# Performance work log

Measured on AMD Instinct MI355X. Metric: run time of the kernel, lower is better.

Reference implementation:

```python
import jax, jax.numpy as jnp
import numpy as np

LAYER_SIZES = [256, 256, 256, 128]
MAX_PATHS = 100
BATCH = 16


def setup_inputs() -> dict:
    key = jax.random.key(0)
    ks = jax.random.split(key, 20)
    d = {}
    d["x"] = jax.random.normal(ks[0], (BATCH, LAYER_SIZES[0]), dtype=jnp.float32)
    # PathPreservingLayer weights W_l: [out, in]
    for l in range(3):
        fi, fo = LAYER_SIZES[l], LAYER_SIZES[l + 1]
        d[f"W{l}"] = jax.random.normal(ks[1 + l], (fo, fi), dtype=jnp.float32) / np.sqrt(fi)
        # quality scorer for layer l: Linear(fo,32) -> ReLU -> Linear(32,1)
        kk = jax.random.split(ks[4 + l], 4)
        d[f"s{l}_w1"] = jax.random.normal(kk[0], (32, fo), dtype=jnp.float32) / np.sqrt(fo)
        d[f"s{l}_b1"] = jnp.zeros((32,), dtype=jnp.float32)
        d[f"s{l}_w2"] = jax.random.normal(kk[1], (1, 32), dtype=jnp.float32) / np.sqrt(32.0)
        d[f"s{l}_b2"] = jnp.zeros((1,), dtype=jnp.float32)
    return d


def _path_layer(data, W):
    # data: [B, Fin, P]; W: [Fout, Fin]
    # path-preserving expansion: new[b, j, p*Fin + i] = W[j, i] * data[b, i, p]
    B, I, P = data.shape
    O = W.shape[0]
    out = jnp.einsum("oi,bip->bopi", W, data)  # [B, O, P, I]
    return out.reshape(B, O, P * I)


def _score(data, w1, b1, w2, b2):
    # data: [B, F, P] -> scores [B, P] via tiny MLP over feature dim per path
    t = jnp.swapaxes(data, 1, 2)  # [B, P, F]
    h = jax.nn.relu(jnp.einsum("bpf,hf->bph", t, w1) + b1)
    return (jnp.einsum("bph,oh->bpo", h, w2) + b2)[..., 0]


def _prune(data, scores, keep):
    _, idx = jax.lax.top_k(scores, keep)  # [B, keep]
    return jnp.take_along_axis(data, idx[:, None, :], axis=-1)


def reference(x, W0, W1, W2,
              s0_w1, s0_b1, s0_w2, s0_b2,
              s1_w1, s1_b1, s1_w2, s1_b2,
              s2_w1, s2_b1, s2_w2, s2_b2):
    Ws = [W0, W1, W2]
    scorers = [(s0_w1, s0_b1, s0_w2, s0_b2),
               (s1_w1, s1_b1, s1_w2, s1_b2),
               (s2_w1, s2_b1, s2_w2, s2_b2)]
    data = x[..., None]  # [B, F0, 1]
    n = len(Ws)
    for i in range(n):
        data = _path_layer(data, Ws[i])
        if data.shape[-1] > MAX_PATHS:
            sc = _score(data, *scorers[i])
            data = _prune(data, sc, MAX_PATHS)
        if i < n - 1:
            data = jnp.tanh(data)
    # quality-weighted output with the last scorer
    w = jax.nn.softmax(_score(data, *scorers[-1]), axis=-1)  # [B, P]
    return jnp.sum(data * w[:, None, :], axis=-1)  # [B, F_last]
```

## Files before the change

kernel.cpp:

```cpp
#include <hip/hip_runtime.h>
#include <math.h>

#define NT 1024
#define KSEL 100
#define NWAVE 16
#define HPAD 260

#define OFF_CT   0
#define OFF_A    24576
#define OFF_B    25344
#define OFF_W0T  26112
#define OFF_W1T  91648
#define OFF_W2T  157184
#define WS_FLOATS 189952

__device__ __forceinline__ unsigned fkey(float f) {
  unsigned u = __float_as_uint(f);
  return (u & 0x80000000u) ? ~u : (u | 0x80000000u);
}
__device__ __forceinline__ float unfkey(unsigned k) {
  return __uint_as_float((k & 0x80000000u) ? (k & 0x7FFFFFFFu) : ~k);
}
__device__ __forceinline__ unsigned long long lower_mask(int lane) {
  return lane ? (~0ull >> (64 - lane)) : 0ull;
}

__device__ __forceinline__ void scan_step(const unsigned* hb, int ncopies, int lane,
                                          int& krem, unsigned& prefix) {
  const int l4 = lane << 2;
  unsigned h0 = 0, h1 = 0, h2 = 0, h3 = 0;
  #pragma unroll 2
  for (int k = 0; k < ncopies; ++k) {
    const uint4 v = *(const uint4*)&hb[k * HPAD + l4];
    h0 += v.x; h1 += v.y; h2 += v.z; h3 += v.w;
  }
  unsigned csum = h0 + h1 + h2 + h3;
  unsigned S = csum;
  #pragma unroll
  for (int off = 1; off < 64; off <<= 1) {
    unsigned v = __shfl_down(S, off, 64);
    if (lane + off < 64) S += v;
  }
  unsigned tail = S - csum;
  unsigned s3 = tail + h3;
  unsigned s2 = s3 + h2;
  unsigned s1 = s2 + h1;
  unsigned s0v = s1 + h0;
  int ld = -1; unsigned sfx = 0, hd = 0;
  if      ((int)s3  >= krem) { ld = l4 + 3; sfx = s3;  hd = h3; }
  else if ((int)s2  >= krem) { ld = l4 + 2; sfx = s2;  hd = h2; }
  else if ((int)s1  >= krem) { ld = l4 + 1; sfx = s1;  hd = h1; }
  else if ((int)s0v >= krem) { ld = l4 + 0; sfx = s0v; hd = h0; }
  int gd = ld;
  #pragma unroll
  for (int off = 32; off >= 1; off >>= 1) {
    int v = __shfl_down(gd, off, 64);
    if (lane + off < 64) gd = (v > gd) ? v : gd;
  }
  gd = __shfl(gd, 0, 64);
  unsigned osfx = __shfl(sfx, gd >> 2, 64);
  unsigned ohd  = __shfl(hd,  gd >> 2, 64);
  krem -= (int)(osfx - ohd);
  prefix = (prefix << 8) | (unsigned)gd;
}

__global__ __launch_bounds__(256) void pqn_precompute(
    const float* __restrict__ W0, const float* __restrict__ W1, const float* __restrict__ W2,
    const float* __restrict__ s0w1, const float* __restrict__ s1w1, const float* __restrict__ s2w1,
    float* __restrict__ ws)
{
  __shared__ float tile[64][65];
  const int bx = blockIdx.x, t = threadIdx.x;
  if (bx < 96) {
    int id = bx * 256 + t;
    int l = id >> 13, r = id & 8191;
    int h = r >> 8, i = r & 255;
    const float* W  = (l == 0) ? W0 : (l == 1) ? W1 : W2;
    const float* w1 = (l == 0) ? s0w1 : (l == 1) ? s1w1 : s2w1;
    float acc = 0.f;
    if (l == 2) {
      #pragma unroll 32
      for (int j = 0; j < 128; ++j)
        acc = fmaf(w1[h * 128 + j], W[j * 256 + i], acc);
    } else {
      #pragma unroll 32
      for (int j = 0; j < 256; ++j)
        acc = fmaf(w1[h * 256 + j], W[j * 256 + i], acc);
    }
    ws[OFF_CT + l * 8192 + h * 256 + i] = acc;
  } else {
    int tb = bx - 96;
    const float* W; float* WT; int R, tbl;
    if (tb < 16)      { W = W0; WT = ws + OFF_W0T; R = 256; tbl = tb; }
    else if (tb < 32) { W = W1; WT = ws + OFF_W1T; R = 256; tbl = tb - 16; }
    else              { W = W2; WT = ws + OFF_W2T; R = 128; tbl = tb - 32; }
    int tr = tbl >> 2, tc = tbl & 3;
    int c = t & 63, r0 = t >> 6;
    #pragma unroll
    for (int k = 0; k < 16; ++k) {
      int r = r0 + (k << 2);
      tile[r][c] = W[(tr * 64 + r) * 256 + tc * 64 + c];
    }
    __syncthreads();
    int r2 = t & 63;
    #pragma unroll
    for (int k = 0; k < 16; ++k) {
      int c2 = r0 + (k << 2);
      WT[(tc * 64 + c2) * R + tr * 64 + r2] = tile[r2][c2];
    }
  }
}

__global__ __launch_bounds__(256) void pqn_ab(
    const float* __restrict__ s0w2, const float* __restrict__ s1w2, const float* __restrict__ s2w2,
    float* __restrict__ ws)
{
  const int l = blockIdx.x;
  const int i = threadIdx.x;
  const float* w2 = (l == 0) ? s0w2 : (l == 1) ? s1w2 : s2w2;
  const float* ct = ws + OFF_CT + l * 8192;
  float a = 0.f, bn = 0.f;
  #pragma unroll
  for (int h = 0; h < 32; ++h) {
    float c = ct[h * 256 + i];
    float wc = w2[h] * c;
    if (c > 0.f) a += wc; else if (c < 0.f) bn += wc;
  }
  ws[OFF_A + l * 256 + i] = a;
  ws[OFF_B + l * 256 + i] = bn;
}

__device__ __forceinline__ float slow_c(const float* __restrict__ w1,
                                        const float* __restrict__ W,
                                        int Fout, int h, int i) {
  float c = 0.f;
  for (int j = 0; j < Fout; ++j) c = fmaf(w1[h * Fout + j], W[j * 256 + i], c);
  return c;
}

__global__ __launch_bounds__(NT) void pqn_main(
    const float* __restrict__ x,
    const float* __restrict__ W0, const float* __restrict__ W1, const float* __restrict__ W2,
    const float* __restrict__ s0w1, const float* __restrict__ s1w1, const float* __restrict__ s2w1,
    const float* __restrict__ s0b1, const float* __restrict__ s1b1, const float* __restrict__ s2b1,
    const float* __restrict__ s0w2, const float* __restrict__ s1w2, const float* __restrict__ s2w2,
    const float* __restrict__ s0b2, const float* __restrict__ s1b2, const float* __restrict__ s2b2,
    const float* __restrict__ wsr,
    float* __restrict__ out)
{
  __shared__ __align__(16) unsigned keyLds[25 * NT];
  __shared__ __align__(16) unsigned hist0[NWAVE * HPAD];
  __shared__ __align__(16) unsigned histP[6 * HPAD];
  __shared__ float Asm[256], Bsm[256];
  __shared__ int   path_col[KSEL]; __shared__ float path_t[KSEL];
  __shared__ int   sel_col[KSEL];  __shared__ float sel_s[KSEL]; __shared__ float sel_sc[KSEL];
  __shared__ unsigned tieq[128];
  __shared__ int nsel_s, ntie_s;
  __shared__ int bz_sh[3];
  __shared__ float wts[KSEL];
  __shared__ float partial[8][128];

  const int b = blockIdx.x;
  const int t = threadIdx.x;
  const int lane = t & 63;
  const int w = t >> 6;
  const bool useWs = (wsr != nullptr);
  const float* Ag  = useWs ? (wsr + OFF_A) : nullptr;
  const float* Bg  = useWs ? (wsr + OFF_B) : nullptr;
  const float* Ctg = useWs ? (wsr + OFF_CT) : nullptr;
  const float* W0T = useWs ? (wsr + OFF_W0T) : nullptr;
  const float* W1T = useWs ? (wsr + OFF_W1T) : nullptr;
  const float* W2T = useWs ? (wsr + OFF_W2T) : nullptr;

  if (!useWs) {
    if (t < 256) {
      float a = 0.f, bn = 0.f;
      for (int h = 0; h < 32; ++h) {
        float c = slow_c(s0w1, W0, 256, h, t);
        float wc = s0w2[h] * c;
        if (c > 0.f) a += wc; else if (c < 0.f) bn += wc;
      }
      Asm[t] = a; Bsm[t] = bn;
    }
    __syncthreads();
  }
  if (w == 0) {
    {
      float v0 = (lane < 32) ? s0b1[lane] : 0.f;
      float v1 = (lane < 32) ? s1b1[lane] : 0.f;
      float v2 = (lane < 32) ? s2b1[lane] : 0.f;
      bz_sh[0] = (__ballot(v0 != 0.f) == 0ull);
      bz_sh[1] = (__ballot(v1 != 0.f) == 0ull);
      bz_sh[2] = (__ballot(v2 != 0.f) == 0ull);
    }
    const bool bz0 = (bz_sh[0] != 0);
    const float b2v = s0b2[0];
    const float4 xv4 = *(const float4*)(x + b * 256 + lane * 4);
    const float xv[4] = {xv4.x, xv4.y, xv4.z, xv4.w};
    float4 A4, B4;
    if (useWs) { A4 = *(const float4*)(Ag + lane * 4); B4 = *(const float4*)(Bg + lane * 4); }
    else       { A4 = *(const float4*)(Asm + lane * 4); B4 = *(const float4*)(Bsm + lane * 4); }
    const float Av[4] = {A4.x, A4.y, A4.z, A4.w};
    const float Bv[4] = {B4.x, B4.y, B4.z, B4.w};
    unsigned kq[4];
    #pragma unroll
    for (int q = 0; q < 4; ++q) {
      int e = 4 * lane + q;
      float s = xv[q];
      float v;
      if (bz0) v = s * (s > 0.f ? Av[q] : Bv[q]) + b2v;
      else {
        v = b2v;
        for (int h = 0; h < 32; ++h) {
          float c = useWs ? Ctg[h * 256 + e] : slow_c(s0w1, W0, 256, h, e);
          v += s0w2[h] * fmaxf(fmaf(s, c, s0b1[h]), 0.f);
        }
      }
      kq[q] = fkey(v);
    }
    int krem = KSEL; unsigned prefix = 0u;
    #pragma unroll
    for (int pass = 0; pass < 4; ++pass) {
      unsigned* hw = (pass == 0) ? hist0 : (histP + (pass - 1) * 2 * HPAD);
      const int l4 = lane << 2;
      hw[l4] = 0u; hw[l4 + 1] = 0u; hw[l4 + 2] = 0u; hw[l4 + 3] = 0u;
      const int shift = 24 - 8 * pass;
      #pragma unroll
      for (int q = 0; q < 4; ++q) {
        bool cand = (pass == 0) || ((kq[q] >> (shift + 8)) == prefix);
        if (cand) atomicAdd(&hw[(kq[q] >> shift) & 255u], 1u);
      }
      scan_step(hw, 1, lane, krem, prefix);
    }
    const unsigned T = prefix;
    int total = 0, ttot = 0;
    #pragma unroll
    for (int q = 0; q < 4; ++q) {
      int e = 4 * lane + q;
      bool sel = kq[q] > T;
      unsigned long long m = __ballot(sel);
      if (sel) {
        int slot = total + (int)__popcll(m & lower_mask(lane));
        path_col[slot] = e; path_t[slot] = xv[q];
      }
      total += (int)__popcll(m);
      bool tie = (kq[q] == T);
      unsigned long long tm = __ballot(tie);
      if (tie) {
        int ts = ttot + (int)__popcll(tm & lower_mask(lane));
        if (ts < 128) tieq[ts] = (unsigned)e;
      }
      ttot += (int)__popcll(tm);
    }
    if (lane == 0) {
      int m = ttot > 128 ? 128 : ttot;
      for (int a2 = 1; a2 < m; ++a2) {
        unsigned v = tieq[a2]; int c = a2 - 1;
        while (c >= 0 && tieq[c] > v) { tieq[c + 1] = tieq[c]; --c; }
        tieq[c + 1] = v;
      }
    }
    const int kt = KSEL - total;
    if (lane < kt) {
      int e = (int)tieq[lane];
      path_col[total + lane] = e; path_t[total + lane] = x[b * 256 + e];
    }
  }
  __syncthreads();

  for (int l = 1; l < 3; ++l) {
    const float* w1 = (l == 1) ? s1w1 : s2w1;
    const float* b1 = (l == 1) ? s1b1 : s2b1;
    const float* w2 = (l == 1) ? s1w2 : s2w2;
    const float  b2v = (l == 1) ? s1b2[0] : s2b2[0];
    const float* Wl = (l == 1) ? W1 : W2;
    const float* Wprev = (l == 1) ? W0 : W1;
    const float* WTprev = (l == 1) ? W0T : W1T;
    const int Fout = (l == 2) ? 128 : 256;

    const float* Ap; const float* Bp;
    if (useWs) { Ap = Ag + l * 256; Bp = Bg + l * 256; }
    else {
      if (t < 256) {
        float a = 0.f, bn = 0.f;
        for (int h = 0; h < 32; ++h) {
          float c = slow_c(w1, Wl, Fout, h, t);
          float wc = w2[h] * c;
          if (c > 0.f) a += wc; else if (c < 0.f) bn += wc;
        }
        Asm[t] = a; Bsm[t] = bn;
      }
      __syncthreads();
      Ap = Asm; Bp = Bsm;
    }
    const bool bz = (bz_sh[l] != 0);
    const float* ctp = useWs ? (Ctg + l * 8192) : nullptr;

    const int i = t & 255;
    const int pq = t >> 8;
    const float Ai = Ap[i], Bi = Bp[i];
    unsigned* histw0 = hist0 + w * HPAD;
    {
      const int l4 = lane << 2;
      histw0[l4] = 0u; histw0[l4 + 1] = 0u; histw0[l4 + 2] = 0u; histw0[l4 + 3] = 0u;
    }
    for (int id = t; id < 6 * HPAD; id += NT) histP[id] = 0u;
    if (t == 0) { nsel_s = 0; ntie_s = 0; }
    unsigned runD = 0x100u; unsigned runC = 0u;
    if (useWs && bz) {
      #pragma unroll
      for (int g = 0; g < 25; g += 8) {
        float wv[8], tv[8];
        #pragma unroll
        for (int jj = 0; jj < 8; ++jj) {
          if (g + jj < 25) {
            int p = pq + ((g + jj) << 2);
            tv[jj] = path_t[p];
            wv[jj] = WTprev[(path_col[p] << 8) + i];
          }
        }
        #pragma unroll
        for (int jj = 0; jj < 8; ++jj) {
          if (g + jj < 25) {
            float s = tanhf(wv[jj] * tv[jj]);
            float v = s * (s > 0.f ? Ai : Bi) + b2v;
            unsigned k = fkey(v);
            keyLds[(g + jj) * NT + t] = k;
            unsigned d = k >> 24;
            if (d == runD) ++runC;
            else { if (runC) atomicAdd(&histw0[runD], runC); runD = d; runC = 1u; }
          }
        }
      }
    } else {
      #pragma unroll
      for (int g = 0; g < 25; g += 4) {
        float wv[4];
        #pragma unroll
        for (int jj = 0; jj < 4; ++jj) {
          if (g + jj < 25) {
            int p = pq + ((g + jj) << 2);
            wv[jj] = useWs ? WTprev[(path_col[p] << 8) + i]
                           : Wprev[i * 256 + path_col[p]];
          }
        }
        #pragma unroll
        for (int jj = 0; jj < 4; ++jj) {
          if (g + jj < 25) {
            int p = pq + ((g + jj) << 2);
            float s = tanhf(wv[jj] * path_t[p]);
            float v;
            if (bz) v = s * (s > 0.f ? Ai : Bi) + b2v;
            else {
              v = b2v;
              for (int h = 0; h < 32; ++h) {
                float c = useWs ? ctp[h * 256 + i] : slow_c(w1, Wl, Fout, h, i);
                v += w2[h] * fmaxf(fmaf(s, c, b1[h]), 0.f);
              }
            }
            unsigned k = fkey(v);
            keyLds[(g + jj) * NT + t] = k;
            unsigned d = k >> 24;
            if (d == runD) ++runC;
            else { if (runC) atomicAdd(&histw0[runD], runC); runD = d; runC = 1u; }
          }
        }
      }
    }
    if (runC) atomicAdd(&histw0[runD], runC);

    int krem = KSEL; unsigned prefix = 0u;
    #pragma unroll
    for (int pass = 0; pass < 4; ++pass) {
      __syncthreads();
      if (pass == 0) scan_step(hist0, NWAVE, lane, krem, prefix);
      else           scan_step(histP + (pass - 1) * 2 * HPAD, 2, lane, krem, prefix);
      if (pass < 3) {
        unsigned* hn = histP + pass * 2 * HPAD + (w & 1) * HPAD;
        const int shift = 24 - 8 * (pass + 1);
        #pragma unroll
        for (int j = 0; j < 25; ++j) {
          unsigned k = keyLds[j * NT + t];
          if ((k >> (shift + 8)) == prefix)
            atomicAdd(&hn[(k >> shift) & 255u], 1u);
        }
      }
    }
    const unsigned T = prefix;

    #pragma unroll
    for (int j = 0; j < 25; ++j) {
      unsigned k = keyLds[j * NT + t];
      int e = j * NT + t;
      if (k > T) {
        int slot = atomicAdd(&nsel_s, 1);
        int p = e >> 8;
        float wq = useWs ? WTprev[(path_col[p] << 8) + i] : Wprev[i * 256 + path_col[p]];
        sel_col[slot] = i;
        sel_s[slot] = tanhf(wq * path_t[p]);
        sel_sc[slot] = unfkey(k);
      } else if (k == T) {
        int tp = atomicAdd(&ntie_s, 1);
        if (tp < 128) tieq[tp] = (unsigned)e;
      }
    }
    __syncthreads();

    if (w == 0) {
      const int G = nsel_s;
      const int kt = KSEL - G;
      if (lane == 0 && kt > 1) {
        int m = ntie_s > 128 ? 128 : ntie_s;
        for (int a2 = 1; a2 < m; ++a2) {
          unsigned v = tieq[a2]; int c = a2 - 1;
          while (c >= 0 && tieq[c] > v) { tieq[c + 1] = tieq[c]; --c; }
          tieq[c + 1] = v;
        }
      }
      if (lane < kt) {
        int e = (int)tieq[lane];
        int ii = e & 255, p = e >> 8;
        float wq = useWs ? WTprev[(path_col[p] << 8) + ii] : Wprev[ii * 256 + path_col[p]];
        sel_col[G + lane] = ii;
        sel_s[G + lane] = tanhf(wq * path_t[p]);
        sel_sc[G + lane] = unfkey(T);
      }
      if (l < 2) {
        if (lane < 64) {
          path_col[lane] = sel_col[lane]; path_t[lane] = sel_s[lane];
          if (lane < 36) { path_col[64 + lane] = sel_col[64 + lane]; path_t[64 + lane] = sel_s[64 + lane]; }
        }
      }
    }
    __syncthreads();
  }

  if (w == 0) {
    float s1v = sel_sc[lane];
    float s2v = (lane < 36) ? sel_sc[64 + lane] : -INFINITY;
    float m = fmaxf(s1v, s2v);
    #pragma unroll
    for (int off = 32; off >= 1; off >>= 1) m = fmaxf(m, __shfl_xor(m, off, 64));
    float e1 = expf(s1v - m);
    float e2 = (lane < 36) ? expf(s2v - m) : 0.f;
    float sv = e1 + e2;
    #pragma unroll
    for (int off = 32; off >= 1; off >>= 1) sv += __shfl_xor(sv, off, 64);
    wts[lane] = e1 * sel_s[lane] / sv;
    if (lane < 36) wts[64 + lane] = e2 * sel_s[64 + lane] / sv;
  }
  __syncthreads();
  {
    const int chunk = w >> 1, half = w & 1;
    const int o = half * 64 + lane;
    const int pb = chunk * 13;
    const int pe = (pb + 13 < KSEL) ? pb + 13 : KSEL;
    float acc = 0.f;
    for (int p = pb; p < pe; ++p) {
      float wq = useWs ? W2T[sel_col[p] * 128 + o] : W2[o * 256 + sel_col[p]];
      acc = fmaf(wq, wts[p], acc);
    }
    partial[chunk][o] = acc;
  }
  __syncthreads();
  if (t < 128) {
    float acc = 0.f;
    #pragma unroll
    for (int c = 0; c < 8; ++c) acc += partial[c][t];
    out[b * 128 + t] = acc;
  }
}

extern "C" void kernel_launch(void* const* d_in, const int* in_sizes, int n_in,
                              void* d_out, int out_size, void* d_ws, size_t ws_size,
                              hipStream_t stream) {
  const float* x    = (const float*)d_in[0];
  const float* W0   = (const float*)d_in[1];
  const float* s0w1 = (const float*)d_in[2];
  const float* s0b1 = (const float*)d_in[3];
  const float* s0w2 = (const float*)d_in[4];
  const float* s0b2 = (const float*)d_in[5];
  const float* W1   = (const float*)d_in[6];
  const float* s1w1 = (const float*)d_in[7];
  const float* s1b1 = (const float*)d_in[8];
  const float* s1w2 = (const float*)d_in[9];
  const float* s1b2 = (const float*)d_in[10];
  const float* W2   = (const float*)d_in[11];
  const float* s2w1 = (const float*)d_in[12];
  const float* s2b1 = (const float*)d_in[13];
  const float* s2w2 = (const float*)d_in[14];
  const float* s2b2 = (const float*)d_in[15];
  float* out = (float*)d_out;
  float* ws  = (float*)d_ws;

  const bool fullWs = ws_size >= (size_t)WS_FLOATS * sizeof(float);
  const float* wsr = nullptr;
  if (fullWs) {
    pqn_precompute<<<136, 256, 0, stream>>>(W0, W1, W2, s0w1, s1w1, s2w1, ws);
    pqn_ab<<<3, 256, 0, stream>>>(s0w2, s1w2, s2w2, ws);
    wsr = ws;
  }
  pqn_main<<<16, NT, 0, stream>>>(x, W0, W1, W2,
                                  s0w1, s1w1, s2w1,
                                  s0b1, s1b1, s2b1,
                                  s0w2, s1w2, s2w2,
                                  s0b2, s1b2, s2b2,
                                  wsr, out);
}
```

Baseline: 150.3 us.

## Compact radix-select candidates and split scorer-weight precompute across more blocks

The radix top-k selection now collects elements matching the 16-bit prefix into a compact LDS candidate list during the second pass, so the last two passes and the final gather scan only the candidates instead of all 25 keys per thread. Elements above the prefix are emitted to the selected set early. Separately, the C = w1·W precompute is split in half along the reduction dimension over twice as many blocks, and the halves are summed in pqn_ab. This adds an overflow fallback path, extra LDS, and an extra workspace layout.

```diff
diff --git a/kernel.cpp b/kernel.cpp
--- a/kernel.cpp
+++ b/kernel.cpp
@@ -5,14 +5,10 @@
 #define KSEL 100
 #define NWAVE 16
 #define HPAD 260
-
-#define OFF_CT   0
-#define OFF_A    24576
-#define OFF_B    25344
-#define OFF_W0T  26112
-#define OFF_W1T  91648
-#define OFF_W2T  157184
-#define WS_FLOATS 189952
+#define CCAP 2048
+
+#define WS_FLOATS_A 239104
+#define WS_FLOATS_B 189952
 
 __device__ __forceinline__ unsigned fkey(float f) {
   unsigned u = __float_as_uint(f);
@@ -67,33 +63,49 @@
 __global__ __launch_bounds__(256) void pqn_precompute(
     const float* __restrict__ W0, const float* __restrict__ W1, const float* __restrict__ W2,
     const float* __restrict__ s0w1, const float* __restrict__ s1w1, const float* __restrict__ s2w1,
-    float* __restrict__ ws)
+    float* __restrict__ ctp0, float* __restrict__ ctp1,
+    float* __restrict__ w0t, float* __restrict__ w1t, float* __restrict__ w2t,
+    int split)
 {
   __shared__ float tile[64][65];
   const int bx = blockIdx.x, t = threadIdx.x;
-  if (bx < 96) {
+  const int ctBlocks = split ? 192 : 96;
+  if (bx < ctBlocks) {
     int id = bx * 256 + t;
-    int l = id >> 13, r = id & 8191;
-    int h = r >> 8, i = r & 255;
+    int l, half, rr;
+    if (split) { l = id >> 14; int r = id & 16383; half = r >> 13; rr = r & 8191; }
+    else       { l = id >> 13; half = 0; rr = id & 8191; }
+    int h = rr >> 8, i = rr & 255;
     const float* W  = (l == 0) ? W0 : (l == 1) ? W1 : W2;
     const float* w1 = (l == 0) ? s0w1 : (l == 1) ? s1w1 : s2w1;
     float acc = 0.f;
-    if (l == 2) {
-      #pragma unroll 32
-      for (int j = 0; j < 128; ++j)
-        acc = fmaf(w1[h * 128 + j], W[j * 256 + i], acc);
+    if (split) {
+      if (l == 2) {
+        int j0 = half * 64;
+        #pragma unroll 32
+        for (int j = j0; j < j0 + 64; ++j)  acc = fmaf(w1[h * 128 + j], W[j * 256 + i], acc);
+      } else {
+        int j0 = half * 128;
+        #pragma unroll 32
+        for (int j = j0; j < j0 + 128; ++j) acc = fmaf(w1[h * 256 + j], W[j * 256 + i], acc);
+      }
+      (half ? ctp1 : ctp0)[l * 8192 + h * 256 + i] = acc;
     } else {
-      #pragma unroll 32
-      for (int j = 0; j < 256; ++j)
-        acc = fmaf(w1[h * 256 + j], W[j * 256 + i], acc);
-    }
-    ws[OFF_CT + l * 8192 + h * 256 + i] = acc;
+      if (l == 2) {
+        #pragma unroll 32
+        for (int j = 0; j < 128; ++j) acc = fmaf(w1[h * 128 + j], W[j * 256 + i], acc);
+      } else {
+        #pragma unroll 32
+        for (int j = 0; j < 256; ++j) acc = fmaf(w1[h * 256 + j], W[j * 256 + i], acc);
+      }
+      ctp0[l * 8192 + h * 256 + i] = acc;
+    }
   } else {
-    int tb = bx - 96;
+    int tb = bx - ctBlocks;
     const float* W; float* WT; int R, tbl;
-    if (tb < 16)      { W = W0; WT = ws + OFF_W0T; R = 256; tbl = tb; }
-    else if (tb < 32) { W = W1; WT = ws + OFF_W1T; R = 256; tbl = tb - 16; }
-    else              { W = W2; WT = ws + OFF_W2T; R = 128; tbl = tb - 32; }
+    if (tb < 16)      { W = W0; WT = w0t; R = 256; tbl = tb; }
+    else if (tb < 32) { W = W1; WT = w1t; R = 256; tbl = tb - 16; }
+    else              { W = W2; WT = w2t; R = 128; tbl = tb - 32; }
     int tr = tbl >> 2, tc = tbl & 3;
     int c = t & 63, r0 = t >> 6;
     #pragma unroll
@@ -113,21 +125,24 @@
 
 __global__ __launch_bounds__(256) void pqn_ab(
     const float* __restrict__ s0w2, const float* __restrict__ s1w2, const float* __restrict__ s2w2,
-    float* __restrict__ ws)
+    const float* __restrict__ ctp0, const float* __restrict__ ctp1,
+    float* __restrict__ ct, float* __restrict__ A, float* __restrict__ B,
+    int split)
 {
   const int l = blockIdx.x;
   const int i = threadIdx.x;
   const float* w2 = (l == 0) ? s0w2 : (l == 1) ? s1w2 : s2w2;
-  const float* ct = ws + OFF_CT + l * 8192;
   float a = 0.f, bn = 0.f;
   #pragma unroll
   for (int h = 0; h < 32; ++h) {
-    float c = ct[h * 256 + i];
+    const int o = l * 8192 + h * 256 + i;
+    float c = ctp0[o];
+    if (split) { c += ctp1[o]; ct[o] = c; }
     float wc = w2[h] * c;
     if (c > 0.f) a += wc; else if (c < 0.f) bn += wc;
   }
-  ws[OFF_A + l * 256 + i] = a;
-  ws[OFF_B + l * 256 + i] = bn;
+  A[l * 256 + i] = a;
+  B[l * 256 + i] = bn;
 }
 
 __device__ __forceinline__ float slow_c(const float* __restrict__ w1,
@@ -145,17 +160,19 @@
     const float* __restrict__ s0b1, const float* __restrict__ s1b1, const float* __restrict__ s2b1,
     const float* __restrict__ s0w2, const float* __restrict__ s1w2, const float* __restrict__ s2w2,
     const float* __restrict__ s0b2, const float* __restrict__ s1b2, const float* __restrict__ s2b2,
-    const float* __restrict__ wsr,
+    const float* __restrict__ Ctg, const float* __restrict__ Ag, const float* __restrict__ Bg,
+    const float* __restrict__ W0T, const float* __restrict__ W1T, const float* __restrict__ W2T,
     float* __restrict__ out)
 {
   __shared__ __align__(16) unsigned keyLds[25 * NT];
   __shared__ __align__(16) unsigned hist0[NWAVE * HPAD];
   __shared__ __align__(16) unsigned histP[6 * HPAD];
+  __shared__ unsigned candK[CCAP]; __shared__ int candE[CCAP];
   __shared__ float Asm[256], Bsm[256];
   __shared__ int   path_col[KSEL]; __shared__ float path_t[KSEL];
   __shared__ int   sel_col[KSEL];  __shared__ float sel_s[KSEL]; __shared__ float sel_sc[KSEL];
   __shared__ unsigned tieq[128];
-  __shared__ int nsel_s, ntie_s;
+  __shared__ int nsel_s, ntie_s, ncand_s;
   __shared__ int bz_sh[3];
   __shared__ float wts[KSEL];
   __shared__ float partial[8][128];
@@ -164,13 +181,7 @@
   const int t = threadIdx.x;
   const int lane = t & 63;
   const int w = t >> 6;
-  const bool useWs = (wsr != nullptr);
-  const float* Ag  = useWs ? (wsr + OFF_A) : nullptr;
-  const float* Bg  = useWs ? (wsr + OFF_B) : nullptr;
-  const float* Ctg = useWs ? (wsr + OFF_CT) : nullptr;
-  const float* W0T = useWs ? (wsr + OFF_W0T) : nullptr;
-  const float* W1T = useWs ? (wsr + OFF_W1T) : nullptr;
-  const float* W2T = useWs ? (wsr + OFF_W2T) : nullptr;
+  const bool useWs = (Ctg != nullptr);
 
   if (!useWs) {
     if (t < 256) {
@@ -305,7 +316,7 @@
       histw0[l4] = 0u; histw0[l4 + 1] = 0u; histw0[l4 + 2] = 0u; histw0[l4 + 3] = 0u;
     }
     for (int id = t; id < 6 * HPAD; id += NT) histP[id] = 0u;
-    if (t == 0) { nsel_s = 0; ntie_s = 0; }
+    if (t == 0) { nsel_s = 0; ntie_s = 0; ncand_s = 0; }
     unsigned runD = 0x100u; unsigned runC = 0u;
     if (useWs && bz) {
       #pragma unroll
@@ -369,39 +380,93 @@
     }
     if (runC) atomicAdd(&histw0[runD], runC);
 
+    __syncthreads();
     int krem = KSEL; unsigned prefix = 0u;
-    #pragma unroll
-    for (int pass = 0; pass < 4; ++pass) {
-      __syncthreads();
-      if (pass == 0) scan_step(hist0, NWAVE, lane, krem, prefix);
-      else           scan_step(histP + (pass - 1) * 2 * HPAD, 2, lane, krem, prefix);
-      if (pass < 3) {
-        unsigned* hn = histP + pass * 2 * HPAD + (w & 1) * HPAD;
-        const int shift = 24 - 8 * (pass + 1);
+    scan_step(hist0, NWAVE, lane, krem, prefix);
+
+    {
+      unsigned* hn = histP + (w & 1) * HPAD;
+      #pragma unroll
+      for (int j = 0; j < 25; ++j) {
+        unsigned k = keyLds[j * NT + t];
+        if ((k >> 24) == prefix) atomicAdd(&hn[(k >> 16) & 255u], 1u);
+      }
+    }
+    __syncthreads();
+    scan_step(histP, 2, lane, krem, prefix);
+
+    {
+      unsigned* hn = histP + 2 * HPAD + (w & 1) * HPAD;
+      #pragma unroll
+      for (int j = 0; j < 25; ++j) {
+        unsigned k = keyLds[j * NT + t];
+        unsigned p16 = k >> 16;
+        if (p16 > prefix) {
+          int slot = atomicAdd(&nsel_s, 1);
+          int e = j * NT + t; int p = e >> 8;
+          float wq = useWs ? WTprev[(path_col[p] << 8) + i] : Wprev[i * 256 + path_col[p]];
+          sel_col[slot] = i; sel_s[slot] = tanhf(wq * path_t[p]); sel_sc[slot] = unfkey(k);
+        } else if (p16 == prefix) {
+          int ci = atomicAdd(&ncand_s, 1);
+          if (ci < CCAP) { candK[ci] = k; candE[ci] = j * NT + t; }
+          atomicAdd(&hn[(k >> 8) & 255u], 1u);
+        }
+      }
+    }
+    __syncthreads();
+    scan_step(histP + 2 * HPAD, 2, lane, krem, prefix);
+    const int ncand = ncand_s;
+    const bool ovf = (ncand > CCAP);
+
+    {
+      unsigned* hn = histP + 4 * HPAD + (w & 1) * HPAD;
+      if (!ovf) {
+        for (int idx = t; idx < ncand; idx += NT) {
+          unsigned k = candK[idx];
+          if ((k >> 8) == prefix) atomicAdd(&hn[k & 255u], 1u);
+        }
+      } else {
         #pragma unroll
         for (int j = 0; j < 25; ++j) {
           unsigned k = keyLds[j * NT + t];
-          if ((k >> (shift + 8)) == prefix)
-            atomicAdd(&hn[(k >> shift) & 255u], 1u);
-        }
-      }
-    }
+          if ((k >> 8) == prefix) atomicAdd(&hn[k & 255u], 1u);
+        }
+      }
+    }
+    __syncthreads();
+    scan_step(histP + 4 * HPAD, 2, lane, krem, prefix);
     const unsigned T = prefix;
 
-    #pragma unroll
-    for (int j = 0; j < 25; ++j) {
-      unsigned k = keyLds[j * NT + t];
-      int e = j * NT + t;
-      if (k > T) {
-        int slot = atomicAdd(&nsel_s, 1);
-        int p = e >> 8;
-        float wq = useWs ? WTprev[(path_col[p] << 8) + i] : Wprev[i * 256 + path_col[p]];
-        sel_col[slot] = i;
-        sel_s[slot] = tanhf(wq * path_t[p]);
-        sel_sc[slot] = unfkey(k);
-      } else if (k == T) {
-        int tp = atomicAdd(&ntie_s, 1);
-        if (tp < 128) tieq[tp] = (unsigned)e;
+    if (!ovf) {
+      for (int idx = t; idx < ncand; idx += NT) {
+        unsigned k = candK[idx];
+        if (k > T) {
+          int e = candE[idx];
+          int slot = atomicAdd(&nsel_s, 1);
+          int ii = e & 255, p = e >> 8;
+          float wq = useWs ? WTprev[(path_col[p] << 8) + ii] : Wprev[ii * 256 + path_col[p]];
+          sel_col[slot] = ii; sel_s[slot] = tanhf(wq * path_t[p]); sel_sc[slot] = unfkey(k);
+        } else if (k == T) {
+          int tp = atomicAdd(&ntie_s, 1);
+          if (tp < 128) tieq[tp] = (unsigned)candE[idx];
+        }
+      }
+    } else {
+      #pragma unroll
+      for (int j = 0; j < 25; ++j) {
+        unsigned k = keyLds[j * NT + t];
+        if ((k >> 16) == (T >> 16)) {
+          int e = j * NT + t;
+          if (k > T) {
+            int slot = atomicAdd(&nsel_s, 1);
+            int p = e >> 8;
+            float wq = useWs ? WTprev[(path_col[p] << 8) + i] : Wprev[i * 256 + path_col[p]];
+            sel_col[slot] = i; sel_s[slot] = tanhf(wq * path_t[p]); sel_sc[slot] = unfkey(k);
+          } else if (k == T) {
+            int tp = atomicAdd(&ntie_s, 1);
+            if (tp < 128) tieq[tp] = (unsigned)e;
+          }
+        }
       }
     }
     __syncthreads();
@@ -493,17 +558,33 @@
   float* out = (float*)d_out;
   float* ws  = (float*)d_ws;
 
-  const bool fullWs = ws_size >= (size_t)WS_FLOATS * sizeof(float);
-  const float* wsr = nullptr;
-  if (fullWs) {
-    pqn_precompute<<<136, 256, 0, stream>>>(W0, W1, W2, s0w1, s1w1, s2w1, ws);
-    pqn_ab<<<3, 256, 0, stream>>>(s0w2, s1w2, s2w2, ws);
-    wsr = ws;
+  const size_t wsf = ws_size / sizeof(float);
+  float *ctp0 = nullptr, *ctp1 = nullptr, *ct = nullptr, *A = nullptr, *B = nullptr;
+  float *w0t = nullptr, *w1t = nullptr, *w2t = nullptr;
+  int split = 0; bool haveWs = false;
+
+  if (wsf >= WS_FLOATS_A) {
+    split = 1; haveWs = true;
+    ctp0 = ws;            ctp1 = ws + 24576;  ct = ws + 49152;
+    A = ws + 73728;       B = ws + 74496;
+    w0t = ws + 75264;     w1t = ws + 140800;  w2t = ws + 206336;
+  } else if (wsf >= WS_FLOATS_B) {
+    split = 0; haveWs = true;
+    ct = ws; ctp0 = ws;   ctp1 = nullptr;
+    A = ws + 24576;       B = ws + 25344;
+    w0t = ws + 26112;     w1t = ws + 91648;   w2t = ws + 157184;
+  }
+
+  if (haveWs) {
+    pqn_precompute<<<split ? 232 : 136, 256, 0, stream>>>(
+        W0, W1, W2, s0w1, s1w1, s2w1, ctp0, ctp1, w0t, w1t, w2t, split);
+    pqn_ab<<<3, 256, 0, stream>>>(s0w2, s1w2, s2w2, ctp0, ctp1, ct, A, B, split);
   }
   pqn_main<<<16, NT, 0, stream>>>(x, W0, W1, W2,
                                   s0w1, s1w1, s2w1,
                                   s0b1, s1b1, s2b1,
                                   s0w2, s1w2, s2w2,
                                   s0b2, s1b2, s2b2,
-                                  wsr, out);
-}
+                                  haveWs ? ct : nullptr, A, B, w0t, w1t, w2t,
+                                  out);
+}
```

Result: no change. 153.0 us (+1.8%).
